# Kernel optimization log

Measured on AMD Instinct MI355X. Metric: run time of the kernel, lower is better.

Reference implementation:

```python
import jax, jax.numpy as jnp
import numpy as np

T = 2048          # tokens (single causal prefill sequence)
H = 4096          # hidden_size
NH = 32           # num query heads
NKV = 8           # num kv heads (GQA)
HD = H // NH      # head_dim = 128
ROPE_THETA = 500000.0
Q_SIZE = NH * HD
KV_SIZE = NKV * HD


def setup_inputs() -> dict:
    key = jax.random.key(0)
    k1, k2, k3 = jax.random.split(key, 3)
    return {
        "positions": jnp.arange(T, dtype=jnp.int32),
        "hidden_states": jax.random.normal(k1, (T, H), dtype=jnp.float32) * 0.02,
        "w_qkv": jax.random.normal(k2, (H, Q_SIZE + 2 * KV_SIZE), dtype=jnp.float32) * (1.0 / np.sqrt(H)),
        "w_o": jax.random.normal(k3, (Q_SIZE, H), dtype=jnp.float32) * (1.0 / np.sqrt(Q_SIZE)),
    }


def _apply_rope(x, positions):
    # x: [T, heads, HD]; neox-style (non-interleaved) RoPE as in get_rope
    half = HD // 2
    inv_freq = 1.0 / (ROPE_THETA ** (jnp.arange(0, half, dtype=jnp.float32) / half * 1.0))
    # note: standard llama uses arange(0, HD, 2)/HD == arange(half)/half
    freqs = positions.astype(jnp.float32)[:, None] * inv_freq[None, :]   # [T, half]
    cos = jnp.cos(freqs)[:, None, :]  # [T, 1, half]
    sin = jnp.sin(freqs)[:, None, :]
    x1, x2 = x[..., :half], x[..., half:]
    return jnp.concatenate([x1 * cos - x2 * sin, x2 * cos + x1 * sin], axis=-1).astype(x.dtype)


def reference(positions, hidden_states, w_qkv, w_o):
    # qkv_proj (no bias)
    qkv = hidden_states @ w_qkv                               # [T, 6144]
    q, k, v = jnp.split(qkv, [Q_SIZE, Q_SIZE + KV_SIZE], axis=-1)
    q = q.reshape(T, NH, HD)
    k = k.reshape(T, NKV, HD)
    v = v.reshape(T, NKV, HD)

    # fused RoPE on q and k (k would be written rotated into the KV cache)
    q = _apply_rope(q, positions)
    k = _apply_rope(k, positions)

    # GQA: expand kv heads to query heads
    group = NH // NKV
    k_rep = jnp.repeat(k, group, axis=1)                      # [T, NH, HD]
    v_rep = jnp.repeat(v, group, axis=1)

    scale = HD ** -0.5
    scores = jnp.einsum('qhd,shd->hqs', q, k_rep) * scale     # [NH, T, T]
    causal = jnp.tril(jnp.ones((T, T), dtype=bool))
    scores = jnp.where(causal[None], scores, jnp.finfo(scores.dtype).min)
    probs = jax.nn.softmax(scores, axis=-1)
    attn = jnp.einsum('hqs,shd->qhd', probs, v_rep)           # [T, NH, HD]

    out = attn.reshape(T, Q_SIZE) @ w_o                       # o_proj
    return out
```

## Files before the change

### kernel.cpp

```cpp
#include <hip/hip_runtime.h>
#include <cstdint>
#include <cstddef>

#define T_SEQ 2048
#define H_DIM 4096
#define NH 32
#define NKV 8
#define HD 128
#define QKV_N 6144
#define Q_SIZE 4096
#define KV_SIZE 1024

typedef __attribute__((ext_vector_type(8))) short bf16x8;
typedef __attribute__((ext_vector_type(4))) short short4v;
typedef __attribute__((ext_vector_type(4))) float f32x4;

__device__ __forceinline__ short f2bf(float f) {
  union { float f; uint32_t u; } v; v.f = f;
  uint32_t r = v.u + 0x7fffu + ((v.u >> 16) & 1u);
  return (short)(r >> 16);
}

__device__ __forceinline__ void gload_lds16(const void* g, void* l) {
  __builtin_amdgcn_global_load_lds((const __attribute__((address_space(1))) void*)g,
                                   (__attribute__((address_space(3))) void*)l,
                                   16, 0, 0);
}

__global__ __launch_bounds__(256) void cvt_bf16_kernel(const float* __restrict__ in,
                                                       short* __restrict__ out, int n4) {
  int i = blockIdx.x * 256 + threadIdx.x;
  if (i < n4) {
    float4 v = ((const float4*)in)[i];
    short4v s;
    s.x = f2bf(v.x); s.y = f2bf(v.y); s.z = f2bf(v.z); s.w = f2bf(v.w);
    ((short4v*)out)[i] = s;
  }
}

__global__ __launch_bounds__(256) void transpose_cvt64_kernel(const float* __restrict__ in,
                                                              short* __restrict__ out,
                                                              int rows, int cols) {
  __shared__ float tile[64][65];
  int bx = blockIdx.x * 64;
  int by = blockIdx.y * 64;
  int t = threadIdx.x;
  int lr = t >> 4;
  int lc4 = t & 15;
#pragma unroll
  for (int p = 0; p < 4; ++p) {
    int r = p * 16 + lr;
    float4 v = *(const float4*)(in + (size_t)(by + r) * cols + bx + lc4 * 4);
    tile[r][lc4 * 4 + 0] = v.x; tile[r][lc4 * 4 + 1] = v.y;
    tile[r][lc4 * 4 + 2] = v.z; tile[r][lc4 * 4 + 3] = v.w;
  }
  __syncthreads();
  int w = t >> 6, l = t & 63;
  int colg = l >> 3;
  int rseg = (l & 7) * 8;
#pragma unroll
  for (int p = 0; p < 2; ++p) {
    int col = (p * 4 + w) * 8 + colg;
    bf16x8 r8;
#pragma unroll
    for (int i = 0; i < 8; ++i) r8[i] = f2bf(tile[rseg + i][col]);
    *(bf16x8*)(out + (size_t)(bx + col) * rows + by + rseg) = r8;
  }
}

#define BARRIER() do { __builtin_amdgcn_s_barrier(); \
                       __builtin_amdgcn_sched_barrier(0); \
                       asm volatile("" ::: "memory"); } while (0)
#define PRIO1 __builtin_amdgcn_s_setprio(1)
#define PRIO0 __builtin_amdgcn_s_setprio(0)

#define VMCNTN() do { \
  if constexpr (NF == 2) asm volatile("s_waitcnt vmcnt(4)" ::: "memory"); \
  else                   asm volatile("s_waitcnt vmcnt(6)" ::: "memory"); } while (0)

#define LDA_HALF(BASE, MH) do { \
  _Pragma("unroll") \
  for (int m_ = 0; m_ < MF; ++m_) { \
    _Pragma("unroll") \
    for (int ks_ = 0; ks_ < 2; ++ks_) { \
      int row_ = arow + (MH) * (WM / 2) + m_ * 16 + l16; \
      aF[m_][ks_] = *(const bf16x8*)((BASE) + row_ * 64 + (((ks_ * 4 + quad) ^ (row_ & 7)) << 3)); \
    } } } while (0)

#define LDB_HALF(BASE, NHH, DST) do { \
  _Pragma("unroll") \
  for (int n_ = 0; n_ < NF; ++n_) { \
    _Pragma("unroll") \
    for (int ks_ = 0; ks_ < 2; ++ks_) { \
      int row_ = brow + (NHH) * (WN / 2) + n_ * 16 + l16; \
      (DST)[n_][ks_] = *(const bf16x8*)((BASE) + row_ * 64 + (((ks_ * 4 + quad) ^ (row_ & 7)) << 3)); \
    } } } while (0)

#define MMQ(MH, NHH, BF) do { \
  _Pragma("unroll") \
  for (int m_ = 0; m_ < MF; ++m_) { \
    _Pragma("unroll") \
    for (int n_ = 0; n_ < NF; ++n_) { \
      _Pragma("unroll") \
      for (int ks_ = 0; ks_ < 2; ++ks_) \
        acc[(MH) * MF + m_][(NHH) * NF + n_] = __builtin_amdgcn_mfma_f32_16x16x32_bf16( \
            aF[m_][ks_], (BF)[n_][ks_], acc[(MH) * MF + m_][(NHH) * NF + n_], 0, 0, 0); \
    } } } while (0)

template<int L>
__device__ __forceinline__ void stage_half(const short* __restrict__ src, int ldk,
                                           short* dst, int half, int tid) {
#pragma unroll
  for (int q = 0; q < L; ++q) {
    int cc = half * (512 * L) + q * 512 + tid;
    int row = cc >> 3, cq = cc & 7;
    gload_lds16(src + (size_t)row * ldk + ((cq ^ (row & 7)) << 3), dst + cc * 8);
  }
}

template<int WM, int WN>
__global__ __launch_bounds__(512, 1) void gemm_bt256_kernel(const short* __restrict__ A,
                                                            const short* __restrict__ Bt,
                                                            float* __restrict__ C,
                                                            int M, int N, int K) {
  constexpr int MF = WM / 32;
  constexpr int NF = WN / 32;
  constexpr int AL = WM / 64;
  constexpr int ASH = 2 * WM * 64;
  constexpr int BSH = 4 * WN * 64;
  __shared__ short lds[2 * (ASH + BSH)];
  short* As0 = lds;
  short* Bs0 = lds + ASH;
  short* As1 = Bs0 + BSH;
  short* Bs1 = As1 + ASH;
  int tid = threadIdx.x;
  int w = tid >> 6, lane = tid & 63;
  int quad = lane >> 4, l16 = lane & 15;
  int wr = w >> 2, wc = w & 3;
  int arow = wr * WM, brow = wc * WN;
  int bm = blockIdx.y * (2 * WM), bn = blockIdx.x * (4 * WN);
  const short* Asrc = A + (size_t)bm * K;
  const short* Bsrc = Bt + (size_t)bn * K;
  int NT = K >> 6, NI = NT >> 1;

  f32x4 acc[2 * MF][2 * NF] = {};
  bf16x8 aF[MF][2], b0F[NF][2], b1F[NF][2];

  stage_half<AL>(Asrc, K, As0, 0, tid);
  stage_half<AL>(Asrc, K, As0, 1, tid);
  stage_half<NF>(Bsrc, K, Bs0, 0, tid);
  stage_half<NF>(Bsrc, K, Bs0, 1, tid);
  stage_half<NF>(Bsrc + 64, K, Bs1, 0, tid);
  stage_half<NF>(Bsrc + 64, K, Bs1, 1, tid);
  VMCNTN();
  BARRIER();

#pragma unroll 1
  for (int i = 0; i < NI; ++i) {
    const short* a1 = Asrc + (size_t)(2 * i + 1) * 64;
    int kt2 = 2 * i + 2; if (kt2 > NT - 1) kt2 = NT - 1;
    int kt3 = 2 * i + 3; if (kt3 > NT - 1) kt3 = NT - 1;
    const short* a2 = Asrc + (size_t)kt2 * 64;
    const short* b2 = Bsrc + (size_t)kt2 * 64;
    const short* b3 = Bsrc + (size_t)kt3 * 64;

    LDA_HALF(As0, 0);
    LDB_HALF(Bs0, 0, b0F);
    stage_half<AL>(a1, K, As1, 0, tid);
    BARRIER();
    PRIO1; MMQ(0, 0, b0F); PRIO0;
    BARRIER();
    LDB_HALF(Bs0, 1, b1F);
    stage_half<AL>(a1, K, As1, 1, tid);
    BARRIER();
    PRIO1; MMQ(0, 1, b1F); PRIO0;
    BARRIER();
    LDA_HALF(As0, 1);
    stage_half<NF>(b2, K, Bs0, 0, tid);
    BARRIER();
    PRIO1; MMQ(1, 1, b1F); PRIO0;
    BARRIER();
    stage_half<NF>(b2, K, Bs0, 1, tid);
    BARRIER();
    PRIO1; MMQ(1, 0, b0F); PRIO0;
    VMCNTN();
    BARRIER();
    LDA_HALF(As1, 0);
    LDB_HALF(Bs1, 0, b0F);
    stage_half<AL>(a2, K, As0, 0, tid);
    BARRIER();
    PRIO1; MMQ(0, 0, b0F); PRIO0;
    BARRIER();
    LDB_HALF(Bs1, 1, b1F);
    stage_half<AL>(a2, K, As0, 1, tid);
    BARRIER();
    PRIO1; MMQ(0, 1, b1F); PRIO0;
    BARRIER();
    LDA_HALF(As1, 1);
    stage_half<NF>(b3, K, Bs1, 0, tid);
    BARRIER();
    PRIO1; MMQ(1, 1, b1F); PRIO0;
    BARRIER();
    stage_half<NF>(b3, K, Bs1, 1, tid);
    BARRIER();
    PRIO1; MMQ(1, 0, b0F); PRIO0;
    VMCNTN();
    BARRIER();
  }
  asm volatile("s_waitcnt vmcnt(0)" ::: "memory");

#pragma unroll
  for (int mi = 0; mi < 2 * MF; ++mi)
#pragma unroll
    for (int ni = 0; ni < 2 * NF; ++ni) {
      int r0 = bm + arow + mi * 16 + quad * 4;
      int c0 = bn + brow + ni * 16 + l16;
#pragma unroll
      for (int r = 0; r < 4; ++r)
        C[(size_t)(r0 + r) * N + c0] = acc[mi][ni][r];
    }
}

__global__ __launch_bounds__(256) void rope_kernel(const float* __restrict__ qkv,
                                                   const int* __restrict__ positions,
                                                   short* __restrict__ qb,
                                                   short* __restrict__ kb) {
  int t = blockIdx.x;
  int hh = blockIdx.y * 4 + (threadIdx.x >> 6);
  int j = threadIdx.x & 63;
  float pos = (float)positions[t];
  float f = pos * exp2f(-(float)j * 0.29580575889569017f);
  float c = cosf(f), sn = sinf(f);
  size_t rowbase = (size_t)t * QKV_N;
  int coloff = (hh < NH) ? hh * HD : Q_SIZE + (hh - NH) * HD;
  float x1 = qkv[rowbase + coloff + j];
  float x2 = qkv[rowbase + coloff + j + 64];
  float o1 = x1 * c - x2 * sn;
  float o2 = x2 * c + x1 * sn;
  const float scale2 = 0.08838834764831845f * 1.4426950408889634f;
  short* dst;
  if (hh < NH) {
    o1 *= scale2; o2 *= scale2;
    dst = qb + ((size_t)hh * T_SEQ + t) * HD;
  } else {
    dst = kb + ((size_t)(hh - NH) * T_SEQ + t) * HD;
  }
  dst[j] = f2bf(o1);
  dst[j + 64] = f2bf(o2);
}

__global__ __launch_bounds__(256) void transpose_v_kernel(const float* __restrict__ qkv,
                                                          short* __restrict__ vt) {
  __shared__ float tile[32][33];
  int bx = blockIdx.x * 32;
  int by = blockIdx.y * 32;
  int x = threadIdx.x, y = threadIdx.y;
#pragma unroll
  for (int i = 0; i < 32; i += 8)
    tile[y + i][x] = qkv[(size_t)(by + y + i) * QKV_N + (Q_SIZE + KV_SIZE) + bx + x];
  __syncthreads();
#pragma unroll
  for (int i = 0; i < 32; i += 8)
    vt[(size_t)(bx + y + i) * T_SEQ + by + x] = f2bf(tile[x][y + i]);
}

#define PS_STR 72
__global__ __launch_bounds__(256, 2) void flash_kernel(const short* __restrict__ qb,
                                                       const short* __restrict__ kb,
                                                       const short* __restrict__ vt,
                                                       short* __restrict__ attn) {
  __shared__ short Ks[64 * 128];
  __shared__ short Vs[128 * 64];
  __shared__ short Ps[8][16 * PS_STR];
  int c = (int)gridDim.x - 1 - (int)blockIdx.x;
  int h = blockIdx.y;
  int kvh = h >> 2;
  int tid = threadIdx.x;
  int w = tid >> 6, lane = tid & 63;
  int quad = lane >> 4, l16 = lane & 15;
  int qrow0w = c * 128 + w * 32;

  const short* kbh = kb + (size_t)kvh * T_SEQ * HD;
  const short* vth = vt + (size_t)kvh * HD * T_SEQ;

  bf16x8 qf[2][4];
#pragma unroll
  for (int g = 0; g < 2; ++g) {
    const short* qbase = qb + ((size_t)h * T_SEQ + qrow0w + g * 16 + l16) * HD + quad * 8;
#pragma unroll
    for (int dk = 0; dk < 4; ++dk) qf[g][dk] = *(const bf16x8*)(qbase + dk * 32);
  }
  f32x4 o[2][8] = {};
  float lp[2] = {0.0f, 0.0f};

  int ktmax_blk = 2 * c + 2;
  int ktmax_w = 2 * c + 1 + (w >> 1);

  for (int kt = 0; kt < ktmax_blk; ++kt) {
    int kpos0 = kt * 64;
    __syncthreads();
#pragma unroll
    for (int p4 = 0; p4 < 4; ++p4) {
      int e = p4 * 256 + tid;
      int kr = e >> 4, kp = e & 15;
      gload_lds16(kbh + (size_t)(kpos0 + kr) * HD + ((kp ^ (kr & 7)) * 8), Ks + e * 8);
      int vd = e >> 3, vp = e & 7;
      gload_lds16(vth + (size_t)vd * T_SEQ + kpos0 + ((vp ^ (vd & 7)) * 8), Vs + e * 8);
    }
    __syncthreads();
    if (kt >= ktmax_w) continue;

    f32x4 s[2][4] = {};
#pragma unroll
    for (int mi = 0; mi < 4; ++mi) {
      int kr = mi * 16 + l16;
      const short* kfb = Ks + kr * 128;
      int sw = kr & 7;
#pragma unroll
      for (int dk = 0; dk < 4; ++dk) {
        bf16x8 kf = *(const bf16x8*)(kfb + (((dk * 4 + quad) ^ sw) * 8));
        s[0][mi] = __builtin_amdgcn_mfma_f32_16x16x32_bf16(kf, qf[0][dk], s[0][mi], 0, 0, 0);
        s[1][mi] = __builtin_amdgcn_mfma_f32_16x16x32_bf16(kf, qf[1][dk], s[1][mi], 0, 0, 0);
      }
    }
#pragma unroll
    for (int g = 0; g < 2; ++g) {
      int qr = qrow0w + g * 16 + l16;
      bool need_mask = (kpos0 + 63 > qrow0w + g * 16);
#pragma unroll
      for (int mi = 0; mi < 4; ++mi) {
        float p0, p1, p2, p3;
        if (need_mask) {
          int kp = kpos0 + mi * 16 + quad * 4;
          p0 = exp2f((kp + 0 > qr) ? -1e30f : s[g][mi][0]);
          p1 = exp2f((kp + 1 > qr) ? -1e30f : s[g][mi][1]);
          p2 = exp2f((kp + 2 > qr) ? -1e30f : s[g][mi][2]);
          p3 = exp2f((kp + 3 > qr) ? -1e30f : s[g][mi][3]);
        } else {
          p0 = exp2f(s[g][mi][0]); p1 = exp2f(s[g][mi][1]);
          p2 = exp2f(s[g][mi][2]); p3 = exp2f(s[g][mi][3]);
        }
        lp[g] += p0 + p1 + p2 + p3;
        short4v pk;
        pk.x = f2bf(p0); pk.y = f2bf(p1); pk.z = f2bf(p2); pk.w = f2bf(p3);
        *(short4v*)(&Ps[w * 2 + g][l16 * PS_STR + mi * 16 + quad * 4]) = pk;
      }
    }
#pragma unroll
    for (int kf2 = 0; kf2 < 2; ++kf2) {
      bf16x8 pf0 = *(const bf16x8*)(&Ps[w * 2 + 0][l16 * PS_STR + kf2 * 32 + quad * 8]);
      bf16x8 pf1 = *(const bf16x8*)(&Ps[w * 2 + 1][l16 * PS_STR + kf2 * 32 + quad * 8]);
#pragma unroll
      for (int ni = 0; ni < 8; ++ni) {
        int vd = ni * 16 + l16;
        bf16x8 vf = *(const bf16x8*)(Vs + vd * 64 + (((kf2 * 4 + quad) ^ (vd & 7)) * 8));
        o[0][ni] = __builtin_amdgcn_mfma_f32_16x16x32_bf16(vf, pf0, o[0][ni], 0, 0, 0);
        o[1][ni] = __builtin_amdgcn_mfma_f32_16x16x32_bf16(vf, pf1, o[1][ni], 0, 0, 0);
      }
    }
  }
#pragma unroll
  for (int g = 0; g < 2; ++g) {
    float lt = lp[g];
    lt += __shfl_xor(lt, 16, 64);
    lt += __shfl_xor(lt, 32, 64);
    float rl = 1.0f / lt;
    short* dst = attn + (size_t)(qrow0w + g * 16 + l16) * Q_SIZE + h * HD + quad * 4;
#pragma unroll
    for (int ni = 0; ni < 8; ++ni) {
      short4v ov;
      ov.x = f2bf(o[g][ni][0] * rl); ov.y = f2bf(o[g][ni][1] * rl);
      ov.z = f2bf(o[g][ni][2] * rl); ov.w = f2bf(o[g][ni][3] * rl);
      *(short4v*)(dst + ni * 16) = ov;
    }
  }
}

extern "C" void kernel_launch(void* const* d_in, const int* in_sizes, int n_in,
                              void* d_out, int out_size, void* d_ws, size_t ws_size,
                              hipStream_t stream) {
  const int* positions = (const int*)d_in[0];
  const float* hidden  = (const float*)d_in[1];
  const float* w_qkv   = (const float*)d_in[2];
  const float* w_o     = (const float*)d_in[3];
  float* out = (float*)d_out;

  char* p = (char*)d_ws;
  short* hA    = (short*)p;               short* attn = hA;
  p += (size_t)T_SEQ * H_DIM * 2;
  short* wqkvT = (short*)p;
  p += (size_t)QKV_N * H_DIM * 2;
  float* qkv   = (float*)p;               short* woT = (short*)p;
  short* qb = wqkvT;
  short* kb = qb + (size_t)NH * T_SEQ * HD;
  short* vt = kb + (size_t)NKV * T_SEQ * HD;

  cvt_bf16_kernel<<<dim3(T_SEQ * H_DIM / 4 / 256), 256, 0, stream>>>(hidden, hA, T_SEQ * H_DIM / 4);
  transpose_cvt64_kernel<<<dim3(QKV_N / 64, H_DIM / 64), 256, 0, stream>>>(w_qkv, wqkvT, H_DIM, QKV_N);
  gemm_bt256_kernel<64, 96><<<dim3(QKV_N / 384, T_SEQ / 128), 512, 0, stream>>>(hA, wqkvT, qkv, T_SEQ, QKV_N, H_DIM);
  rope_kernel<<<dim3(T_SEQ, (NH + NKV) / 4), 256, 0, stream>>>(qkv, positions, qb, kb);
  transpose_v_kernel<<<dim3(KV_SIZE / 32, T_SEQ / 32), dim3(32, 8), 0, stream>>>(qkv, vt);
  transpose_cvt64_kernel<<<dim3(H_DIM / 64, H_DIM / 64), 256, 0, stream>>>(w_o, woT, H_DIM, H_DIM);
  flash_kernel<<<dim3(T_SEQ / 128, NH), 256, 0, stream>>>(qb, kb, vt, attn);
  gemm_bt256_kernel<64, 64><<<dim3(H_DIM / 256, T_SEQ / 128), 512, 0, stream>>>(attn, woT, out, T_SEQ, H_DIM, H_DIM);
}
```

Before: 488.3 us.

## Double-buffer GEMM register fragments and overlap LDS reads with MFMA

Splits the A and B register fragments into two sets each, so the next quarter's LDS reads are issued before the current quarter's MFMAs run instead of after a barrier. A new, looser vmcnt wait replaces the single end-of-half wait, and the first fragments are preloaded before the loop. The aim is to hide LDS read latency behind matrix math in both GEMMs. In exchange it raises register pressure, and the changed wait placement risks reading LDS tiles before their global-to-LDS loads have landed.

```diff
diff --git a/kernel.cpp b/kernel.cpp
--- a/kernel.cpp
+++ b/kernel.cpp
@@ -78,13 +78,17 @@
   if constexpr (NF == 2) asm volatile("s_waitcnt vmcnt(4)" ::: "memory"); \
   else                   asm volatile("s_waitcnt vmcnt(6)" ::: "memory"); } while (0)
 
-#define LDA_HALF(BASE, MH) do { \
+#define VMCNTB() do { \
+  if constexpr (NF == 2) asm volatile("s_waitcnt vmcnt(2)" ::: "memory"); \
+  else                   asm volatile("s_waitcnt vmcnt(3)" ::: "memory"); } while (0)
+
+#define LDA_HALF(BASE, MH, DST) do { \
   _Pragma("unroll") \
   for (int m_ = 0; m_ < MF; ++m_) { \
     _Pragma("unroll") \
     for (int ks_ = 0; ks_ < 2; ++ks_) { \
       int row_ = arow + (MH) * (WM / 2) + m_ * 16 + l16; \
-      aF[m_][ks_] = *(const bf16x8*)((BASE) + row_ * 64 + (((ks_ * 4 + quad) ^ (row_ & 7)) << 3)); \
+      (DST)[m_][ks_] = *(const bf16x8*)((BASE) + row_ * 64 + (((ks_ * 4 + quad) ^ (row_ & 7)) << 3)); \
     } } } while (0)
 
 #define LDB_HALF(BASE, NHH, DST) do { \
@@ -96,7 +100,7 @@
       (DST)[n_][ks_] = *(const bf16x8*)((BASE) + row_ * 64 + (((ks_ * 4 + quad) ^ (row_ & 7)) << 3)); \
     } } } while (0)
 
-#define MMQ(MH, NHH, BF) do { \
+#define MMQ(MH, NHH, AF, BF) do { \
   _Pragma("unroll") \
   for (int m_ = 0; m_ < MF; ++m_) { \
     _Pragma("unroll") \
@@ -104,7 +108,7 @@
       _Pragma("unroll") \
       for (int ks_ = 0; ks_ < 2; ++ks_) \
         acc[(MH) * MF + m_][(NHH) * NF + n_] = __builtin_amdgcn_mfma_f32_16x16x32_bf16( \
-            aF[m_][ks_], (BF)[n_][ks_], acc[(MH) * MF + m_][(NHH) * NF + n_], 0, 0, 0); \
+            (AF)[m_][ks_], (BF)[n_][ks_], acc[(MH) * MF + m_][(NHH) * NF + n_], 0, 0, 0); \
     } } } while (0)
 
 template<int L>
@@ -144,7 +148,7 @@
   int NT = K >> 6, NI = NT >> 1;
 
   f32x4 acc[2 * MF][2 * NF] = {};
-  bf16x8 aF[MF][2], b0F[NF][2], b1F[NF][2];
+  bf16x8 aA[MF][2], aB[MF][2], bA[NF][2], bB[NF][2];
 
   stage_half<AL>(Asrc, K, As0, 0, tid);
   stage_half<AL>(Asrc, K, As0, 1, tid);
@@ -154,6 +158,8 @@
   stage_half<NF>(Bsrc + 64, K, Bs1, 1, tid);
   VMCNTN();
   BARRIER();
+  LDA_HALF(As0, 0, aA);
+  LDB_HALF(Bs0, 0, bA);
 
 #pragma unroll 1
   for (int i = 0; i < NI; ++i) {
@@ -164,47 +170,47 @@
     const short* b2 = Bsrc + (size_t)kt2 * 64;
     const short* b3 = Bsrc + (size_t)kt3 * 64;
 
-    LDA_HALF(As0, 0);
-    LDB_HALF(Bs0, 0, b0F);
     stage_half<AL>(a1, K, As1, 0, tid);
     BARRIER();
-    PRIO1; MMQ(0, 0, b0F); PRIO0;
-    BARRIER();
-    LDB_HALF(Bs0, 1, b1F);
+    LDB_HALF(Bs0, 1, bB);
+    PRIO1; MMQ(0, 0, aA, bA); PRIO0;
+    BARRIER();
     stage_half<AL>(a1, K, As1, 1, tid);
     BARRIER();
-    PRIO1; MMQ(0, 1, b1F); PRIO0;
-    BARRIER();
-    LDA_HALF(As0, 1);
+    LDA_HALF(As0, 1, aB);
+    PRIO1; MMQ(0, 1, aA, bB); PRIO0;
+    BARRIER();
     stage_half<NF>(b2, K, Bs0, 0, tid);
-    BARRIER();
-    PRIO1; MMQ(1, 1, b1F); PRIO0;
+    VMCNTB();
+    BARRIER();
+    PRIO1; MMQ(1, 1, aB, bB); PRIO0;
     BARRIER();
     stage_half<NF>(b2, K, Bs0, 1, tid);
     BARRIER();
-    PRIO1; MMQ(1, 0, b0F); PRIO0;
-    VMCNTN();
-    BARRIER();
-    LDA_HALF(As1, 0);
-    LDB_HALF(Bs1, 0, b0F);
+    PRIO1; MMQ(1, 0, aB, bA); PRIO0;
+    LDA_HALF(As1, 0, aA);
+    LDB_HALF(Bs1, 0, bA);
+    BARRIER();
     stage_half<AL>(a2, K, As0, 0, tid);
     BARRIER();
-    PRIO1; MMQ(0, 0, b0F); PRIO0;
-    BARRIER();
-    LDB_HALF(Bs1, 1, b1F);
+    LDB_HALF(Bs1, 1, bB);
+    PRIO1; MMQ(0, 0, aA, bA); PRIO0;
+    BARRIER();
     stage_half<AL>(a2, K, As0, 1, tid);
     BARRIER();
-    PRIO1; MMQ(0, 1, b1F); PRIO0;
-    BARRIER();
-    LDA_HALF(As1, 1);
+    LDA_HALF(As1, 1, aB);
+    PRIO1; MMQ(0, 1, aA, bB); PRIO0;
+    BARRIER();
     stage_half<NF>(b3, K, Bs1, 0, tid);
-    BARRIER();
-    PRIO1; MMQ(1, 1, b1F); PRIO0;
+    VMCNTB();
+    BARRIER();
+    PRIO1; MMQ(1, 1, aB, bB); PRIO0;
     BARRIER();
     stage_half<NF>(b3, K, Bs1, 1, tid);
     BARRIER();
-    PRIO1; MMQ(1, 0, b0F); PRIO0;
-    VMCNTN();
+    PRIO1; MMQ(1, 0, aB, bA); PRIO0;
+    LDA_HALF(As0, 0, aA);
+    LDB_HALF(Bs0, 0, bA);
     BARRIER();
   }
   asm volatile("s_waitcnt vmcnt(0)" ::: "memory");
```

Result: no change. 492.6 us (+0.9%).
